# Kernel tuning notes

Hardware: AMD Instinct MI355X
Metric: run time of the kernel (lower is better)

The kernel has to match this reference:

```python
import jax, jax.numpy as jnp
import numpy as np
import math

B, DSET, DOUT, DH, H, L, M, C = 32, 512, 16, 1024, 16, 6, 127, 8
S = M + 1            # sos + maximum_components targets
DHEAD = DH // H
DIN = DSET + 1 + 2 * DOUT  # embedding input dim = 545
DTOK = 1 + 2 * DOUT        # per-step token dim = 33


def _pos_encoding(max_len, d):
    pos = np.arange(max_len, dtype=np.float32)[:, None]
    div = np.exp(np.arange(0, d, 2, dtype=np.float32) * (-math.log(10000.0) / d))
    pe = np.zeros((max_len, d), dtype=np.float32)
    pe[:, 0::2] = np.sin(pos * div)
    pe[:, 1::2] = np.cos(pos * div)
    return jnp.asarray(pe[None])  # [1, max_len, d]


def setup_inputs() -> dict:
    key = jax.random.key(0)
    ks = iter(jax.random.split(key, 64))
    def n(shape, s=0.02):
        return jax.random.normal(next(ks), shape, jnp.float32) * s
    return {
        "input": jax.random.normal(next(ks), (B, DSET), jnp.float32),
        "targets": jax.random.normal(next(ks), (B, M, DTOK), jnp.float32),
        "W_emb": n((DH, DIN)), "b_emb": jnp.zeros((DH,), jnp.float32),
        "sos": jax.random.normal(next(ks), (1, 1, DTOK), jnp.float32),
        "Wqkv": n((L, 3 * DH, DH)), "bqkv": jnp.zeros((L, 3 * DH), jnp.float32),
        "Wo": n((L, DH, DH)), "bo": jnp.zeros((L, DH), jnp.float32),
        "W1": n((L, DH, DH)), "b1": jnp.zeros((L, DH), jnp.float32),
        "W2": n((L, DH, DH)), "b2": jnp.zeros((L, DH), jnp.float32),
        "g1": jnp.ones((L, DH), jnp.float32), "be1": jnp.zeros((L, DH), jnp.float32),
        "g2": jnp.ones((L, DH), jnp.float32), "be2": jnp.zeros((L, DH), jnp.float32),
        "Wm": n((1, DH)), "bm": jnp.zeros((1,), jnp.float32),
        "Wpi_m": n((C, DH)), "bpi_m": jnp.zeros((C,), jnp.float32),
        "Wmu_m": n((C * DOUT, DH)), "bmu_m": jnp.zeros((C * DOUT,), jnp.float32),
        "Wsg_m": n((C * DOUT, DH)), "bsg_m": jnp.zeros((C * DOUT,), jnp.float32),
        "Wpi_v": n((C, DH)), "bpi_v": jnp.zeros((C,), jnp.float32),
        "Wmu_v": n((C * DOUT, DH)), "bmu_v": jnp.zeros((C * DOUT,), jnp.float32),
        "Wsg_v": n((C * DOUT, DH)), "bsg_v": jnp.zeros((C * DOUT,), jnp.float32),
    }


def _ln(x, g, b, eps=1e-5):
    m = x.mean(-1, keepdims=True)
    v = ((x - m) ** 2).mean(-1, keepdims=True)
    return (x - m) / jnp.sqrt(v + eps) * g + b


def _layer(x, Wqkv, bqkv, Wo, bo, W1, b1, W2, b2, g1, be1, g2, be2, causal):
    # PyTorch TransformerEncoderLayer (post-norm, relu, dropout=0)
    qkv = x @ Wqkv.T + bqkv                       # [B,S,3*DH]
    q, k, v = jnp.split(qkv, 3, axis=-1)
    q = q.reshape(B, -1, H, DHEAD)
    k = k.reshape(B, -1, H, DHEAD)
    v = v.reshape(B, -1, H, DHEAD)
    sc = jnp.einsum('bqhd,bkhd->bhqk', q, k) / math.sqrt(DHEAD)
    sc = jnp.where(causal, sc, -1e30)
    a = jax.nn.softmax(sc, -1)
    o = jnp.einsum('bhqk,bkhd->bqhd', a, v).reshape(B, -1, DH)
    x = _ln(x + o @ Wo.T + bo, g1, be1)
    ff = jax.nn.relu(x @ W1.T + b1) @ W2.T + b2
    return _ln(x + ff, g2, be2)


def _mdn(h, Wpi, bpi, Wmu, bmu, Wsg, bsg):
    pi = jax.nn.softmax(h @ Wpi.T + bpi, -1)                      # [B,M,C]
    mu = (h @ Wmu.T + bmu).reshape(h.shape[:-1] + (C, DOUT))      # [B,M,C,DOUT]
    var = jnp.exp(h @ Wsg.T + bsg).reshape(h.shape[:-1] + (C, DOUT))
    return pi, mu, var


def reference(input, targets, W_emb, b_emb, sos, Wqkv, bqkv, Wo, bo, W1, b1, W2, b2,
              g1, be1, g2, be2, Wm, bm, Wpi_m, bpi_m, Wmu_m, bmu_m, Wsg_m, bsg_m,
              Wpi_v, bpi_v, Wmu_v, bmu_v, Wsg_v, bsg_v):
    pe = _pos_encoding(3 * M, DH)
    tokens = jnp.broadcast_to(sos, (B, 1, DTOK))
    cond = jnp.broadcast_to(input[:, None, :], (B, S, DSET))
    seq = jnp.concatenate([tokens, targets], axis=1)              # [B,S,DTOK]
    x = jnp.concatenate([cond, seq], axis=-1) @ W_emb.T + b_emb
    x = x + pe[:, :S, :]
    causal = jnp.tril(jnp.ones((S, S), bool))[None, None]
    for i in range(L):
        x = _layer(x, Wqkv[i], bqkv[i], Wo[i], bo[i], W1[i], b1[i], W2[i], b2[i],
                   g1[i], be1[i], g2[i], be2[i], causal)
    h = x[:, :-1, :]                                              # [B,M,DH]
    masks = h @ Wm.T + bm                                         # [B,M,1]
    pi_m, mu_m, var_m = _mdn(h, Wpi_m, bpi_m, Wmu_m, bmu_m, Wsg_m, bsg_m)
    pi_v, mu_v, var_v = _mdn(h, Wpi_v, bpi_v, Wmu_v, bmu_v, Wsg_v, bsg_v)
    return (pi_m, mu_m, var_m, pi_v, mu_v, var_v, masks)
```

## Files before the change

### kernel.cpp

```cpp
#include <hip/hip_runtime.h>
#include <hip/hip_bf16.h>

typedef __hip_bfloat16 bf16;
typedef __attribute__((ext_vector_type(8))) short bfrag8;
typedef __attribute__((ext_vector_type(4))) float facc4;
typedef __attribute__((ext_vector_type(4))) unsigned short us4;
typedef __attribute__((ext_vector_type(8))) unsigned short us8;
typedef __attribute__((ext_vector_type(4))) float f32x4;

#define AS1C const __attribute__((address_space(1))) void
#define AS3  __attribute__((address_space(3))) void

__device__ __forceinline__ void gload_lds16(const void* src, void* dst) {
    __builtin_amdgcn_global_load_lds((AS1C*)src, (AS3*)dst, 16, 0, 0);
}

__device__ __forceinline__ unsigned short f2bf(float f) {
    unsigned u = __float_as_uint(f);
    unsigned r = u + 0x7FFFu + ((u >> 16) & 1u);
    return (unsigned short)(r >> 16);
}
__device__ __forceinline__ float bf2f(unsigned short u) {
    return __uint_as_float((unsigned)u << 16);
}

__global__ void prep_cvt_kernel(const float* __restrict__ input, const float* __restrict__ targets,
                                const float* __restrict__ sos, const float* __restrict__ W_emb,
                                const float* __restrict__ Wm, const float* __restrict__ Wpi_m,
                                const float* __restrict__ Wmu_m, const float* __restrict__ Wsg_m,
                                const float* __restrict__ Wpi_v, const float* __restrict__ Wmu_v,
                                const float* __restrict__ Wsg_v,
                                const float* __restrict__ bm, const float* __restrict__ bpi_m,
                                const float* __restrict__ bmu_m, const float* __restrict__ bsg_m,
                                const float* __restrict__ bpi_v, const float* __restrict__ bmu_v,
                                const float* __restrict__ bsg_v,
                                const float* __restrict__ Wqkv, const float* __restrict__ Wo,
                                const float* __restrict__ W1, const float* __restrict__ W2,
                                float* __restrict__ pe, bf16* __restrict__ xin,
                                bf16* __restrict__ wemb, bf16* __restrict__ whead,
                                float* __restrict__ bhead,
                                bf16* __restrict__ wqb, bf16* __restrict__ wob,
                                bf16* __restrict__ w1b, bf16* __restrict__ w2b) {
    int bid = blockIdx.x;
    if (bid < 4608) {
        int l = bid / 768;
        int s = bid - l * 768;
        const float* src; bf16* dst;
        if (s < 384)      { src = Wqkv + (size_t)l * 3145728; dst = wqb + (size_t)l * 3145728; }
        else if (s < 512) { src = Wo + (size_t)l * 1048576; dst = wob + (size_t)l * 1048576; s -= 384; }
        else if (s < 640) { src = W1 + (size_t)l * 1048576; dst = w1b + (size_t)l * 1048576; s -= 512; }
        else              { src = W2 + (size_t)l * 1048576; dst = w2b + (size_t)l * 1048576; s -= 640; }
        size_t pbase = (size_t)s * 1024 + threadIdx.x;
#pragma unroll
        for (int it = 0; it < 4; ++it) {
            size_t o = (pbase + it * 256) * 8;
            const f32x4* p = (const f32x4*)(src + o);
            f32x4 v1 = __builtin_nontemporal_load(p);
            f32x4 v2 = __builtin_nontemporal_load(p + 1);
            us8 w8;
            w8[0] = f2bf(v1.x); w8[1] = f2bf(v1.y); w8[2] = f2bf(v1.z); w8[3] = f2bf(v1.w);
            w8[4] = f2bf(v2.x); w8[5] = f2bf(v2.y); w8[6] = f2bf(v2.z); w8[7] = f2bf(v2.w);
            *(us8*)(dst + o) = w8;
        }
    } else if (bid < 5120) {
        int idx = (bid - 4608) * 256 + threadIdx.x;
        int s = idx >> 10, c = idx & 1023;
        int i = c >> 1;
        float div = expf(-9.210340371976184f * (float)(2 * i) * (1.f / 1024.f));
        float a = (float)s * div;
        pe[idx] = (c & 1) ? cosf(a) : sinf(a);
    } else if (bid < 5120 + 4096) {
        int row = bid - 5120;
        int b = row >> 7, s = row & 127;
        for (int c = threadIdx.x; c < 576; c += 256) {
            float v = 0.f;
            if (c < 512) v = input[b * 512 + c];
            else if (c < 545) {
                int j = c - 512;
                v = (s == 0) ? sos[j] : targets[((size_t)b * 127 + (s - 1)) * 33 + j];
            }
            xin[(size_t)row * 576 + c] = __float2bfloat16(v);
        }
    } else if (bid < 5120 + 4096 + 1024) {
        int row = bid - (5120 + 4096);
        for (int c = threadIdx.x; c < 576; c += 256)
            wemb[(size_t)row * 576 + c] = __float2bfloat16(c < 545 ? W_emb[(size_t)row * 545 + c] : 0.f);
    } else {
        int r = bid - (5120 + 4096 + 1024);
        const float* wsrc = nullptr; const float* bsrc = nullptr; int off = 0;
        if (r == 0)        { wsrc = Wm;    bsrc = bm;    off = 0; }
        else if (r < 9)    { wsrc = Wpi_m; bsrc = bpi_m; off = r - 1; }
        else if (r < 137)  { wsrc = Wmu_m; bsrc = bmu_m; off = r - 9; }
        else if (r < 265)  { wsrc = Wsg_m; bsrc = bsg_m; off = r - 137; }
        else if (r < 273)  { wsrc = Wpi_v; bsrc = bpi_v; off = r - 265; }
        else if (r < 401)  { wsrc = Wmu_v; bsrc = bmu_v; off = r - 273; }
        else if (r < 529)  { wsrc = Wsg_v; bsrc = bsg_v; off = r - 401; }
        for (int c = threadIdx.x; c < 1024; c += 256)
            whead[(size_t)r * 1024 + c] = __float2bfloat16(wsrc ? wsrc[(size_t)off * 1024 + c] : 0.f);
        if (threadIdx.x == 0 && wsrc) bhead[r] = bsrc[off];
    }
}

template<int EPI, int DBUF>
__global__ __launch_bounds__(256, DBUF ? 2 : 3) void gemm_bt(
    const bf16* __restrict__ A, const bf16* __restrict__ Bw,
    float* __restrict__ Cf, bf16* __restrict__ Cb,
    const float* __restrict__ bias, const float* __restrict__ pe,
    int M, int N, int K, int lda, int ldb, int ldc, long long Az, long long Cz)
{
    __shared__ __align__(16) bf16 sA[DBUF ? 2 : 1][128 * 64];
    __shared__ __align__(16) bf16 sB[DBUF ? 2 : 1][128 * 64];
    const int t = threadIdx.x;
    const int w = t >> 6, la = t & 63;
    const int wm = (w >> 1) * 64, wn = (w & 1) * 64;
    const int m0 = blockIdx.y * 128, n0 = blockIdx.x * 128;
    const int z = blockIdx.z;
    A += (long long)z * Az;

    const int c0 = w * 64 + la;
    facc4 zero4 = {0.f, 0.f, 0.f, 0.f};
    facc4 acc[4][4];
#pragma unroll
    for (int mi = 0; mi < 4; ++mi)
#pragma unroll
        for (int ni = 0; ni < 4; ++ni) acc[mi][ni] = zero4;

    auto stage = [&](int buf, int kt) {
#pragma unroll
        for (int i = 0; i < 4; ++i) {
            int c = i * 256 + c0;
            int r = c >> 3;
            int bc = ((c & 7) * 16) ^ ((r & 7) << 4);
            gload_lds16(A + (size_t)(m0 + r) * lda + kt + (bc >> 1),
                        (char*)sA[buf] + (size_t)(i * 256 + c0) * 16);
            gload_lds16(Bw + (size_t)(n0 + r) * ldb + kt + (bc >> 1),
                        (char*)sB[buf] + (size_t)(i * 256 + c0) * 16);
        }
    };
    auto compute = [&](int buf) {
#pragma unroll
        for (int ks = 0; ks < 2; ++ks) {
            bfrag8 af[4], bfv[4];
            const int koffb = (ks * 32 + (la >> 4) * 8) * 2;
#pragma unroll
            for (int i = 0; i < 4; ++i) {
                int rowa = wm + i * 16 + (la & 15);
                af[i] = *(const bfrag8*)((const char*)sA[buf] + rowa * 128 + (koffb ^ ((rowa & 7) << 4)));
                int rowb = wn + i * 16 + (la & 15);
                bfv[i] = *(const bfrag8*)((const char*)sB[buf] + rowb * 128 + (koffb ^ ((rowb & 7) << 4)));
            }
#pragma unroll
            for (int mi = 0; mi < 4; ++mi)
#pragma unroll
                for (int ni = 0; ni < 4; ++ni)
                    acc[mi][ni] = __builtin_amdgcn_mfma_f32_16x16x32_bf16(bfv[ni], af[mi], acc[mi][ni], 0, 0, 0);
        }
    };

    const int nk = K >> 6;
    if constexpr (DBUF) {
        stage(0, 0);
        __syncthreads();
        int cur = 0;
        for (int kt = 0; kt < nk; ++kt) {
            if (kt + 1 < nk) stage(cur ^ 1, (kt + 1) << 6);
            compute(cur);
            __syncthreads();
            cur ^= 1;
        }
    } else {
        for (int kt = 0; kt < nk; ++kt) {
            stage(0, kt << 6);
            __syncthreads();
            compute(0);
            __syncthreads();
        }
    }
#pragma unroll
    for (int mi = 0; mi < 4; ++mi) {
        int row = m0 + wm + mi * 16 + (la & 15);
#pragma unroll
        for (int ni = 0; ni < 4; ++ni) {
            int colb = n0 + wn + ni * 16 + (la >> 4) * 4;
            if constexpr (EPI == 3) {
                if (row >= M) continue;
#pragma unroll
                for (int j = 0; j < 4; ++j) {
                    int col = colb + j;
                    if (col < N)
                        Cf[(size_t)z * Cz + (size_t)row * ldc + col] = acc[mi][ni][j] + bias[col];
                }
            } else {
                float4 bv = *(const float4*)(bias + colb);
                facc4 v = acc[mi][ni];
                v[0] += bv.x; v[1] += bv.y; v[2] += bv.z; v[3] += bv.w;
                size_t cidx = (size_t)row * ldc + colb;
                if constexpr (EPI == 0) {
                    us4 o; o.x = f2bf(v[0]); o.y = f2bf(v[1]); o.z = f2bf(v[2]); o.w = f2bf(v[3]);
                    *(us4*)(Cb + cidx) = o;
                } else if constexpr (EPI == 1) {
                    us4 o;
                    o.x = f2bf(v[0] > 0.f ? v[0] : 0.f); o.y = f2bf(v[1] > 0.f ? v[1] : 0.f);
                    o.z = f2bf(v[2] > 0.f ? v[2] : 0.f); o.w = f2bf(v[3] > 0.f ? v[3] : 0.f);
                    *(us4*)(Cb + cidx) = o;
                } else {
                    float4 p = *(const float4*)(pe + (size_t)(row & 127) * 1024 + colb);
                    us4 o;
                    o.x = f2bf(v[0] + p.x); o.y = f2bf(v[1] + p.y);
                    o.z = f2bf(v[2] + p.z); o.w = f2bf(v[3] + p.w);
                    *(us4*)(Cb + cidx) = o;
                }
            }
        }
    }
}

__global__ __launch_bounds__(256) void attn_fused(const bf16* __restrict__ qkv, bf16* __restrict__ obf)
{
    __shared__ __align__(16) char lds[65536];
    char* sQ  = lds;
    char* sK  = lds + 16384;
    char* sS  = lds + 32768;
    char* sVT = lds;
    float* redm = (float*)(lds + 16384);
    float* reds = (float*)(lds + 16384 + 1024);

    const int t = threadIdx.x, w = t >> 6, la = t & 63;
    const int b = blockIdx.x >> 4, h = blockIdx.x & 15;
    const size_t base = (size_t)b * 128 * 3072 + (size_t)h * 64;

#pragma unroll
    for (int i = 0; i < 4; ++i) {
        int c = i * 256 + w * 64 + la;
        int r = c >> 3;
        int bc = ((c & 7) * 16) ^ ((r & 7) << 4);
        gload_lds16(qkv + base + (size_t)r * 3072 + (bc >> 1),
                    sQ + (size_t)(i * 256 + w * 64) * 16);
        gload_lds16(qkv + base + 1024 + (size_t)r * 3072 + (bc >> 1),
                    sK + (size_t)(i * 256 + w * 64) * 16);
    }
    __syncthreads();

    const int wm = (w >> 1) * 64, wn = (w & 1) * 64;
    facc4 zero4 = {0.f, 0.f, 0.f, 0.f};
    facc4 acc[4][4];
#pragma unroll
    for (int mi = 0; mi < 4; ++mi)
#pragma unroll
        for (int ni = 0; ni < 4; ++ni) acc[mi][ni] = zero4;
#pragma unroll
    for (int ks = 0; ks < 2; ++ks) {
        bfrag8 af[4], bfv[4];
        const int koffb = (ks * 32 + (la >> 4) * 8) * 2;
#pragma unroll
        for (int i = 0; i < 4; ++i) {
            int rowa = wm + i * 16 + (la & 15);
            af[i] = *(const bfrag8*)(sQ + rowa * 128 + (koffb ^ ((rowa & 7) << 4)));
            int rowb = wn + i * 16 + (la & 15);
            bfv[i] = *(const bfrag8*)(sK + rowb * 128 + (koffb ^ ((rowb & 7) << 4)));
        }
#pragma unroll
        for (int mi = 0; mi < 4; ++mi)
#pragma unroll
            for (int ni = 0; ni < 4; ++ni)
                acc[mi][ni] = __builtin_amdgcn_mfma_f32_16x16x32_bf16(bfv[ni], af[mi], acc[mi][ni], 0, 0, 0);
    }
    __syncthreads();

#pragma unroll
    for (int i = 0; i < 4; ++i) {
        int c = i * 256 + t;
        int r = c >> 3;
        int d0 = (c & 7) * 8;
        bfrag8 vv = *(const bfrag8*)(qkv + base + 2048 + (size_t)r * 3072 + d0);
#pragma unroll
        for (int j = 0; j < 8; ++j) {
            int d = d0 + j;
            *(short*)(sVT + d * 256 + ((2 * r) ^ ((d & 7) << 4))) = vv[j];
        }
    }

    const int colh = (w & 1) * 128;
    float tmp4[4];
#pragma unroll
    for (int mi = 0; mi < 4; ++mi) {
        int q = wm + mi * 16 + (la & 15);
        float mx = -1e30f;
#pragma unroll
        for (int ni = 0; ni < 4; ++ni) {
            int kb = wn + ni * 16 + (la >> 4) * 4;
#pragma unroll
            for (int j = 0; j < 4; ++j) {
                float s = acc[mi][ni][j] * 0.125f;
                acc[mi][ni][j] = s;
                if (kb + j <= q) mx = fmaxf(mx, s);
            }
        }
        mx = fmaxf(mx, __shfl_xor(mx, 16));
        mx = fmaxf(mx, __shfl_xor(mx, 32));
        tmp4[mi] = mx;
    }
    if ((la >> 4) == 0) {
#pragma unroll
        for (int mi = 0; mi < 4; ++mi) redm[colh + wm + mi * 16 + la] = tmp4[mi];
    }
    __syncthreads();
#pragma unroll
    for (int mi = 0; mi < 4; ++mi) {
        int q = wm + mi * 16 + (la & 15);
        float m = fmaxf(redm[q], redm[128 + q]);
        float sm = 0.f;
#pragma unroll
        for (int ni = 0; ni < 4; ++ni) {
            int kb = wn + ni * 16 + (la >> 4) * 4;
#pragma unroll
            for (int j = 0; j < 4; ++j) {
                float e = (kb + j <= q) ? __expf(acc[mi][ni][j] - m) : 0.f;
                acc[mi][ni][j] = e;
                sm += e;
            }
        }
        sm += __shfl_xor(sm, 16);
        sm += __shfl_xor(sm, 32);
        tmp4[mi] = sm;
    }
    __syncthreads();
    if ((la >> 4) == 0) {
#pragma unroll
        for (int mi = 0; mi < 4; ++mi) reds[colh + wm + mi * 16 + la] = tmp4[mi];
    }
    __syncthreads();
#pragma unroll
    for (int mi = 0; mi < 4; ++mi) {
        int q = wm + mi * 16 + (la & 15);
        float inv = 1.f / (reds[q] + reds[128 + q]);
#pragma unroll
        for (int ni = 0; ni < 4; ++ni) {
            int kb = wn + ni * 16 + (la >> 4) * 4;
            us4 sv;
            sv.x = f2bf(acc[mi][ni][0] * inv); sv.y = f2bf(acc[mi][ni][1] * inv);
            sv.z = f2bf(acc[mi][ni][2] * inv); sv.w = f2bf(acc[mi][ni][3] * inv);
            *(us4*)(sS + q * 256 + ((2 * kb) ^ ((q & 7) << 4))) = sv;
        }
    }
    __syncthreads();

    const int wm2 = (w >> 1) * 64, wn2 = (w & 1) * 32;
    facc4 a2[4][2];
#pragma unroll
    for (int mi = 0; mi < 4; ++mi) { a2[mi][0] = zero4; a2[mi][1] = zero4; }
#pragma unroll
    for (int ks = 0; ks < 4; ++ks) {
        bfrag8 pa[4], vb[2];
        const int koffb = (ks * 32 + (la >> 4) * 8) * 2;
#pragma unroll
        for (int mi = 0; mi < 4; ++mi) {
            int rowa = wm2 + mi * 16 + (la & 15);
            pa[mi] = *(const bfrag8*)(sS + rowa * 256 + (koffb ^ ((rowa & 7) << 4)));
        }
#pragma unroll
        for (int ni = 0; ni < 2; ++ni) {
            int rowb = wn2 + ni * 16 + (la & 15);
            vb[ni] = *(const bfrag8*)(sVT + rowb * 256 + (koffb ^ ((rowb & 7) << 4)));
        }
#pragma unroll
        for (int mi = 0; mi < 4; ++mi)
#pragma unroll
            for (int ni = 0; ni < 2; ++ni)
                a2[mi][ni] = __builtin_amdgcn_mfma_f32_16x16x32_bf16(vb[ni], pa[mi], a2[mi][ni], 0, 0, 0);
    }
#pragma unroll
    for (int mi = 0; mi < 4; ++mi) {
        int s = wm2 + mi * 16 + (la & 15);
#pragma unroll
        for (int ni = 0; ni < 2; ++ni) {
            int db = wn2 + ni * 16 + (la >> 4) * 4;
            us4 ov;
            ov.x = f2bf(a2[mi][ni][0]); ov.y = f2bf(a2[mi][ni][1]);
            ov.z = f2bf(a2[mi][ni][2]); ov.w = f2bf(a2[mi][ni][3]);
            *(us4*)(obf + ((size_t)(b * 128 + s)) * 1024 + h * 64 + db) = ov;
        }
    }
}

__global__ __launch_bounds__(256) void ln_res_kernel(const bf16* __restrict__ go,
                                                     const bf16* __restrict__ res,
                                                     const float* __restrict__ g, const float* __restrict__ be,
                                                     bf16* __restrict__ xb_out)
{
    const int row = blockIdx.x, t = threadIdx.x;
    size_t o = (size_t)row * 1024 + t * 4;
    us4 gv4 = *(const us4*)(go + o);
    us4 rv4 = *(const us4*)(res + o);
    float t0 = bf2f(rv4.x) + bf2f(gv4.x);
    float t1 = bf2f(rv4.y) + bf2f(gv4.y);
    float t2 = bf2f(rv4.z) + bf2f(gv4.z);
    float t3 = bf2f(rv4.w) + bf2f(gv4.w);
    float s = t0 + t1 + t2 + t3;
    float q = t0 * t0 + t1 * t1 + t2 * t2 + t3 * t3;
#pragma unroll
    for (int off = 32; off; off >>= 1) {
        s += __shfl_xor(s, off);
        q += __shfl_xor(q, off);
    }
    __shared__ float ssum[4], sqs[4];
    if ((t & 63) == 0) { ssum[t >> 6] = s; sqs[t >> 6] = q; }
    __syncthreads();
    s = ssum[0] + ssum[1] + ssum[2] + ssum[3];
    q = sqs[0] + sqs[1] + sqs[2] + sqs[3];
    float mean = s * (1.f / 1024.f);
    float var = q * (1.f / 1024.f) - mean * mean;
    float rstd = rsqrtf(var + 1e-5f);
    float4 gv = *(const float4*)(g + t * 4);
    float4 bv = *(const float4*)(be + t * 4);
    float o0 = (t0 - mean) * rstd * gv.x + bv.x;
    float o1 = (t1 - mean) * rstd * gv.y + bv.y;
    float o2 = (t2 - mean) * rstd * gv.z + bv.z;
    float o3 = (t3 - mean) * rstd * gv.w + bv.w;
    us4 obv; obv.x = f2bf(o0); obv.y = f2bf(o1); obv.z = f2bf(o2); obv.w = f2bf(o3);
    *(us4*)(xb_out + o) = obv;
}

__global__ void finalize_kernel(const float* __restrict__ hout, float* __restrict__ out) {
    const size_t O_PI_M = 0, O_MU_M = 32512, O_VAR_M = 552704, O_PI_V = 1072896,
                 O_MU_V = 1105408, O_VAR_V = 1625600, O_MASK = 2145792;
    int rm = blockIdx.x;
    const float* hrow = hout + (size_t)rm * 529;
    int t = threadIdx.x;
    if (t < 128) {
        out[O_MU_M  + (size_t)rm * 128 + t] = hrow[9 + t];
        out[O_VAR_M + (size_t)rm * 128 + t] = expf(hrow[137 + t]);
        out[O_MU_V  + (size_t)rm * 128 + t] = hrow[273 + t];
        out[O_VAR_V + (size_t)rm * 128 + t] = expf(hrow[401 + t]);
    } else if (t == 128) {
        out[O_MASK + rm] = hrow[0];
    } else if (t == 129 || t == 130) {
        int boff = (t == 129) ? 1 : 265;
        size_t oo = ((t == 129) ? O_PI_M : O_PI_V) + (size_t)rm * 8;
        float v[8], mx = -1e30f;
#pragma unroll
        for (int j = 0; j < 8; ++j) { v[j] = hrow[boff + j]; mx = fmaxf(mx, v[j]); }
        float sm = 0.f;
#pragma unroll
        for (int j = 0; j < 8; ++j) { v[j] = expf(v[j] - mx); sm += v[j]; }
        float inv = 1.f / sm;
#pragma unroll
        for (int j = 0; j < 8; ++j) out[oo + j] = v[j] * inv;
    }
}

extern "C" void kernel_launch(void* const* d_in, const int* in_sizes, int n_in,
                              void* d_out, int out_size, void* d_ws, size_t ws_size,
                              hipStream_t stream) {
    (void)in_sizes; (void)n_in; (void)out_size; (void)ws_size;
    const float* input   = (const float*)d_in[0];
    const float* targets = (const float*)d_in[1];
    const float* W_emb   = (const float*)d_in[2];
    const float* b_emb   = (const float*)d_in[3];
    const float* sos     = (const float*)d_in[4];
    const float* Wqkv    = (const float*)d_in[5];
    const float* bqkv    = (const float*)d_in[6];
    const float* Wo      = (const float*)d_in[7];
    const float* bo      = (const float*)d_in[8];
    const float* W1      = (const float*)d_in[9];
    const float* b1      = (const float*)d_in[10];
    const float* W2      = (const float*)d_in[11];
    const float* b2      = (const float*)d_in[12];
    const float* g1      = (const float*)d_in[13];
    const float* be1     = (const float*)d_in[14];
    const float* g2      = (const float*)d_in[15];
    const float* be2     = (const float*)d_in[16];
    const float* Wm      = (const float*)d_in[17];
    const float* bm      = (const float*)d_in[18];
    const float* Wpi_m   = (const float*)d_in[19];
    const float* bpi_m   = (const float*)d_in[20];
    const float* Wmu_m   = (const float*)d_in[21];
    const float* bmu_m   = (const float*)d_in[22];
    const float* Wsg_m   = (const float*)d_in[23];
    const float* bsg_m   = (const float*)d_in[24];
    const float* Wpi_v   = (const float*)d_in[25];
    const float* bpi_v   = (const float*)d_in[26];
    const float* Wmu_v   = (const float*)d_in[27];
    const float* bmu_v   = (const float*)d_in[28];
    const float* Wsg_v   = (const float*)d_in[29];
    const float* bsg_v   = (const float*)d_in[30];
    float* out = (float*)d_out;

    char* ws = (char*)d_ws;
    float* pe      = (float*)(ws + 0);
    bf16*  xin     = (bf16*)(ws + 524288);
    bf16*  wemb    = (bf16*)(ws + 5242880);
    bf16*  whead   = (bf16*)(ws + 6422528);
    float* bhead   = (float*)(ws + 7733248);
    bf16*  xb      = (bf16*)(ws + 24513024);
    bf16*  qkvb    = (bf16*)(ws + 32901632);
    bf16*  ob      = (bf16*)(ws + 58067456);
    bf16*  tmpb    = (bf16*)(ws + 66456064);
    bf16*  wqb_all = (bf16*)(ws + 83233280);
    bf16*  wob_all = (bf16*)(ws + 120982016);
    bf16*  w1b_all = (bf16*)(ws + 133564928);
    bf16*  w2b_all = (bf16*)(ws + 146147840);
    float* hout    = (float*)(ws + 158730752);

    prep_cvt_kernel<<<10880, 256, 0, stream>>>(input, targets, sos, W_emb,
                                               Wm, Wpi_m, Wmu_m, Wsg_m, Wpi_v, Wmu_v, Wsg_v,
                                               bm, bpi_m, bmu_m, bsg_m, bpi_v, bmu_v, bsg_v,
                                               Wqkv, Wo, W1, W2,
                                               pe, xin, wemb, whead, bhead,
                                               wqb_all, wob_all, w1b_all, w2b_all);
    gemm_bt<4, 1><<<dim3(8, 32, 1), 256, 0, stream>>>(xin, wemb, nullptr, xb, b_emb, pe,
                                                      4096, 1024, 576, 576, 576, 1024, 0, 0);
    for (int l = 0; l < 6; ++l) {
        const bf16* wqb = wqb_all + (size_t)l * 3145728;
        const bf16* wob = wob_all + (size_t)l * 1048576;
        const bf16* w1b = w1b_all + (size_t)l * 1048576;
        const bf16* w2b = w2b_all + (size_t)l * 1048576;
        gemm_bt<0, 0><<<dim3(24, 32, 1), 256, 0, stream>>>(xb, wqb, nullptr, qkvb, bqkv + l * 3072,
                                                           nullptr, 4096, 3072, 1024, 1024, 1024, 3072, 0, 0);
        attn_fused<<<512, 256, 0, stream>>>(qkvb, ob);
        gemm_bt<0, 1><<<dim3(8, 32, 1), 256, 0, stream>>>(ob, wob, nullptr, tmpb, bo + l * 1024,
                                                          nullptr, 4096, 1024, 1024, 1024, 1024, 1024, 0, 0);
        ln_res_kernel<<<4096, 256, 0, stream>>>(tmpb, xb, g1 + l * 1024, be1 + l * 1024, xb);
        gemm_bt<1, 1><<<dim3(8, 32, 1), 256, 0, stream>>>(xb, w1b, nullptr, ob, b1 + l * 1024,
                                                          nullptr, 4096, 1024, 1024, 1024, 1024, 1024, 0, 0);
        gemm_bt<0, 1><<<dim3(8, 32, 1), 256, 0, stream>>>(ob, w2b, nullptr, tmpb, b2 + l * 1024,
                                                          nullptr, 4096, 1024, 1024, 1024, 1024, 1024, 0, 0);
        ln_res_kernel<<<4096, 256, 0, stream>>>(tmpb, xb, g2 + l * 1024, be2 + l * 1024, xb);
    }
    gemm_bt<3, 1><<<dim3(5, 1, 32), 256, 0, stream>>>(xb, whead, hout, nullptr, bhead, nullptr,
                                                      127, 529, 1024, 1024, 1024, 529, 131072LL, 67183LL);
    finalize_kernel<<<4064, 256, 0, stream>>>(hout, out);
}
```

Baseline: 773.9 us.

## Use 512-thread blocks for double-buffered GEMMs and vectorize prep conversion

The double-buffered GEMM now runs 8 waves per 128x128 tile instead of 4. Each wave owns a 32x64 sub-tile, and each thread stages half as many LDS chunks. This is meant to raise latency hiding and the number of active waves per CU for the N=1024 GEMMs, which launch only 256 blocks. The prep kernel is also reworked to do vectorized 8-wide bf16 conversion with fewer blocks and a single block for the head biases, cutting per-element scalar work. More waves per tile means each wave reuses fewer A fragments, so LDS read traffic per MFMA goes up.

```diff
diff --git a/kernel.cpp b/kernel.cpp
--- a/kernel.cpp
+++ b/kernel.cpp
@@ -42,6 +42,7 @@
                                 bf16* __restrict__ wqb, bf16* __restrict__ wob,
                                 bf16* __restrict__ w1b, bf16* __restrict__ w2b) {
     int bid = blockIdx.x;
+    int t = threadIdx.x;
     if (bid < 4608) {
         int l = bid / 768;
         int s = bid - l * 768;
@@ -50,7 +51,7 @@
         else if (s < 512) { src = Wo + (size_t)l * 1048576; dst = wob + (size_t)l * 1048576; s -= 384; }
         else if (s < 640) { src = W1 + (size_t)l * 1048576; dst = w1b + (size_t)l * 1048576; s -= 512; }
         else              { src = W2 + (size_t)l * 1048576; dst = w2b + (size_t)l * 1048576; s -= 640; }
-        size_t pbase = (size_t)s * 1024 + threadIdx.x;
+        size_t pbase = (size_t)s * 1024 + t;
 #pragma unroll
         for (int it = 0; it < 4; ++it) {
             size_t o = (pbase + it * 256) * 8;
@@ -62,95 +63,150 @@
             w8[4] = f2bf(v2.x); w8[5] = f2bf(v2.y); w8[6] = f2bf(v2.z); w8[7] = f2bf(v2.w);
             *(us8*)(dst + o) = w8;
         }
-    } else if (bid < 5120) {
-        int idx = (bid - 4608) * 256 + threadIdx.x;
-        int s = idx >> 10, c = idx & 1023;
-        int i = c >> 1;
-        float div = expf(-9.210340371976184f * (float)(2 * i) * (1.f / 1024.f));
-        float a = (float)s * div;
-        pe[idx] = (c & 1) ? cosf(a) : sinf(a);
-    } else if (bid < 5120 + 4096) {
-        int row = bid - 5120;
+    } else if (bid < 4736) {
+        int s = bid - 4608;
+        float4 v;
+#pragma unroll
+        for (int j = 0; j < 4; ++j) {
+            int c = t * 4 + j;
+            int i = c >> 1;
+            float div = expf(-9.210340371976184f * (float)(2 * i) * (1.f / 1024.f));
+            float a = (float)s * div;
+            v[j] = (c & 1) ? cosf(a) : sinf(a);
+        }
+        *(float4*)(pe + (size_t)s * 1024 + t * 4) = v;
+    } else if (bid < 5888) {
+        int chunk = (bid - 4736) * 256 + t;
+        int row = chunk / 72;
+        int cc = chunk - row * 72;
         int b = row >> 7, s = row & 127;
-        for (int c = threadIdx.x; c < 576; c += 256) {
-            float v = 0.f;
-            if (c < 512) v = input[b * 512 + c];
-            else if (c < 545) {
-                int j = c - 512;
-                v = (s == 0) ? sos[j] : targets[((size_t)b * 127 + (s - 1)) * 33 + j];
+        us8 w8;
+        if (cc < 64) {
+            const float* p = input + (size_t)b * 512 + cc * 8;
+            float4 v1 = *(const float4*)p;
+            float4 v2 = *(const float4*)(p + 4);
+            w8[0] = f2bf(v1.x); w8[1] = f2bf(v1.y); w8[2] = f2bf(v1.z); w8[3] = f2bf(v1.w);
+            w8[4] = f2bf(v2.x); w8[5] = f2bf(v2.y); w8[6] = f2bf(v2.z); w8[7] = f2bf(v2.w);
+        } else {
+#pragma unroll
+            for (int j = 0; j < 8; ++j) {
+                int col = cc * 8 + j;
+                float v = 0.f;
+                if (col < 545) {
+                    int jj = col - 512;
+                    v = (s == 0) ? sos[jj] : targets[((size_t)b * 127 + (s - 1)) * 33 + jj];
+                }
+                w8[j] = f2bf(v);
             }
-            xin[(size_t)row * 576 + c] = __float2bfloat16(v);
-        }
-    } else if (bid < 5120 + 4096 + 1024) {
-        int row = bid - (5120 + 4096);
-        for (int c = threadIdx.x; c < 576; c += 256)
-            wemb[(size_t)row * 576 + c] = __float2bfloat16(c < 545 ? W_emb[(size_t)row * 545 + c] : 0.f);
+        }
+        *(us8*)(xin + (size_t)row * 576 + cc * 8) = w8;
+    } else if (bid < 6176) {
+        int chunk = (bid - 5888) * 256 + t;
+        int row = chunk / 72;
+        int cc = chunk - row * 72;
+        us8 w8;
+#pragma unroll
+        for (int j = 0; j < 8; ++j) {
+            int col = cc * 8 + j;
+            w8[j] = f2bf(col < 545 ? W_emb[(size_t)row * 545 + col] : 0.f);
+        }
+        *(us8*)(wemb + (size_t)row * 576 + cc * 8) = w8;
+    } else if (bid < 6496) {
+        int chunk = (bid - 6176) * 256 + t;
+        int r = chunk >> 7;
+        int cc = chunk & 127;
+        const float* wsrc = nullptr; int off = 0;
+        if (r == 0)        { wsrc = Wm;    off = 0; }
+        else if (r < 9)    { wsrc = Wpi_m; off = r - 1; }
+        else if (r < 137)  { wsrc = Wmu_m; off = r - 9; }
+        else if (r < 265)  { wsrc = Wsg_m; off = r - 137; }
+        else if (r < 273)  { wsrc = Wpi_v; off = r - 265; }
+        else if (r < 401)  { wsrc = Wmu_v; off = r - 273; }
+        else if (r < 529)  { wsrc = Wsg_v; off = r - 401; }
+        us8 w8;
+        if (wsrc) {
+            const float* p = wsrc + (size_t)off * 1024 + cc * 8;
+            float4 v1 = *(const float4*)p;
+            float4 v2 = *(const float4*)(p + 4);
+            w8[0] = f2bf(v1.x); w8[1] = f2bf(v1.y); w8[2] = f2bf(v1.z); w8[3] = f2bf(v1.w);
+            w8[4] = f2bf(v2.x); w8[5] = f2bf(v2.y); w8[6] = f2bf(v2.z); w8[7] = f2bf(v2.w);
+        } else {
+#pragma unroll
+            for (int j = 0; j < 8; ++j) w8[j] = 0;
+        }
+        *(us8*)(whead + (size_t)r * 1024 + cc * 8) = w8;
     } else {
-        int r = bid - (5120 + 4096 + 1024);
-        const float* wsrc = nullptr; const float* bsrc = nullptr; int off = 0;
-        if (r == 0)        { wsrc = Wm;    bsrc = bm;    off = 0; }
-        else if (r < 9)    { wsrc = Wpi_m; bsrc = bpi_m; off = r - 1; }
-        else if (r < 137)  { wsrc = Wmu_m; bsrc = bmu_m; off = r - 9; }
-        else if (r < 265)  { wsrc = Wsg_m; bsrc = bsg_m; off = r - 137; }
-        else if (r < 273)  { wsrc = Wpi_v; bsrc = bpi_v; off = r - 265; }
-        else if (r < 401)  { wsrc = Wmu_v; bsrc = bmu_v; off = r - 273; }
-        else if (r < 529)  { wsrc = Wsg_v; bsrc = bsg_v; off = r - 401; }
-        for (int c = threadIdx.x; c < 1024; c += 256)
-            whead[(size_t)r * 1024 + c] = __float2bfloat16(wsrc ? wsrc[(size_t)off * 1024 + c] : 0.f);
-        if (threadIdx.x == 0 && wsrc) bhead[r] = bsrc[off];
-    }
-}
-
-template<int EPI, int DBUF>
-__global__ __launch_bounds__(256, DBUF ? 2 : 3) void gemm_bt(
+        if (t < 529) {
+            const float* bsrc; int off;
+            if (t == 0)       { bsrc = bm;    off = 0; }
+            else if (t < 9)   { bsrc = bpi_m; off = t - 1; }
+            else if (t < 137) { bsrc = bmu_m; off = t - 9; }
+            else if (t < 265) { bsrc = bsg_m; off = t - 137; }
+            else if (t < 273) { bsrc = bpi_v; off = t - 265; }
+            else if (t < 401) { bsrc = bmu_v; off = t - 273; }
+            else              { bsrc = bsg_v; off = t - 401; }
+            bhead[t] = bsrc[off];
+        }
+    }
+}
+
+template<int EPI, int CFG>
+__global__ __launch_bounds__(CFG ? 512 : 256, CFG ? 2 : 3) void gemm_bt(
     const bf16* __restrict__ A, const bf16* __restrict__ Bw,
     float* __restrict__ Cf, bf16* __restrict__ Cb,
     const float* __restrict__ bias, const float* __restrict__ pe,
     int M, int N, int K, int lda, int ldb, int ldc, long long Az, long long Cz)
 {
-    __shared__ __align__(16) bf16 sA[DBUF ? 2 : 1][128 * 64];
-    __shared__ __align__(16) bf16 sB[DBUF ? 2 : 1][128 * 64];
+    constexpr int NT = CFG ? 512 : 256;
+    constexpr int NB = CFG ? 2 : 1;
+    constexpr int MI = CFG ? 2 : 4;
+    constexpr int NCH = 1024 / NT;
+    __shared__ __align__(16) bf16 sA[NB][128 * 64];
+    __shared__ __align__(16) bf16 sB[NB][128 * 64];
     const int t = threadIdx.x;
     const int w = t >> 6, la = t & 63;
-    const int wm = (w >> 1) * 64, wn = (w & 1) * 64;
+    const int wm = CFG ? (w >> 1) * 32 : (w >> 1) * 64;
+    const int wn = (w & 1) * 64;
     const int m0 = blockIdx.y * 128, n0 = blockIdx.x * 128;
     const int z = blockIdx.z;
     A += (long long)z * Az;
 
-    const int c0 = w * 64 + la;
     facc4 zero4 = {0.f, 0.f, 0.f, 0.f};
-    facc4 acc[4][4];
-#pragma unroll
-    for (int mi = 0; mi < 4; ++mi)
+    facc4 acc[MI][4];
+#pragma unroll
+    for (int mi = 0; mi < MI; ++mi)
 #pragma unroll
         for (int ni = 0; ni < 4; ++ni) acc[mi][ni] = zero4;
 
     auto stage = [&](int buf, int kt) {
 #pragma unroll
-        for (int i = 0; i < 4; ++i) {
-            int c = i * 256 + c0;
+        for (int i = 0; i < NCH; ++i) {
+            int c = i * NT + t;
             int r = c >> 3;
             int bc = ((c & 7) * 16) ^ ((r & 7) << 4);
             gload_lds16(A + (size_t)(m0 + r) * lda + kt + (bc >> 1),
-                        (char*)sA[buf] + (size_t)(i * 256 + c0) * 16);
+                        (char*)sA[buf] + (size_t)c * 16);
             gload_lds16(Bw + (size_t)(n0 + r) * ldb + kt + (bc >> 1),
-                        (char*)sB[buf] + (size_t)(i * 256 + c0) * 16);
+                        (char*)sB[buf] + (size_t)c * 16);
         }
     };
     auto compute = [&](int buf) {
 #pragma unroll
         for (int ks = 0; ks < 2; ++ks) {
-            bfrag8 af[4], bfv[4];
+            bfrag8 af[MI], bfv[4];
             const int koffb = (ks * 32 + (la >> 4) * 8) * 2;
 #pragma unroll
-            for (int i = 0; i < 4; ++i) {
+            for (int i = 0; i < MI; ++i) {
                 int rowa = wm + i * 16 + (la & 15);
                 af[i] = *(const bfrag8*)((const char*)sA[buf] + rowa * 128 + (koffb ^ ((rowa & 7) << 4)));
+            }
+#pragma unroll
+            for (int i = 0; i < 4; ++i) {
                 int rowb = wn + i * 16 + (la & 15);
                 bfv[i] = *(const bfrag8*)((const char*)sB[buf] + rowb * 128 + (koffb ^ ((rowb & 7) << 4)));
             }
 #pragma unroll
-            for (int mi = 0; mi < 4; ++mi)
+            for (int mi = 0; mi < MI; ++mi)
 #pragma unroll
                 for (int ni = 0; ni < 4; ++ni)
                     acc[mi][ni] = __builtin_amdgcn_mfma_f32_16x16x32_bf16(bfv[ni], af[mi], acc[mi][ni], 0, 0, 0);
@@ -158,7 +214,7 @@
     };
 
     const int nk = K >> 6;
-    if constexpr (DBUF) {
+    if constexpr (CFG) {
         stage(0, 0);
         __syncthreads();
         int cur = 0;
@@ -177,7 +233,7 @@
         }
     }
 #pragma unroll
-    for (int mi = 0; mi < 4; ++mi) {
+    for (int mi = 0; mi < MI; ++mi) {
         int row = m0 + wm + mi * 16 + (la & 15);
 #pragma unroll
         for (int ni = 0; ni < 4; ++ni) {
@@ -502,13 +558,13 @@
     bf16*  w2b_all = (bf16*)(ws + 146147840);
     float* hout    = (float*)(ws + 158730752);
 
-    prep_cvt_kernel<<<10880, 256, 0, stream>>>(input, targets, sos, W_emb,
-                                               Wm, Wpi_m, Wmu_m, Wsg_m, Wpi_v, Wmu_v, Wsg_v,
-                                               bm, bpi_m, bmu_m, bsg_m, bpi_v, bmu_v, bsg_v,
-                                               Wqkv, Wo, W1, W2,
-                                               pe, xin, wemb, whead, bhead,
-                                               wqb_all, wob_all, w1b_all, w2b_all);
-    gemm_bt<4, 1><<<dim3(8, 32, 1), 256, 0, stream>>>(xin, wemb, nullptr, xb, b_emb, pe,
+    prep_cvt_kernel<<<6497, 256, 0, stream>>>(input, targets, sos, W_emb,
+                                              Wm, Wpi_m, Wmu_m, Wsg_m, Wpi_v, Wmu_v, Wsg_v,
+                                              bm, bpi_m, bmu_m, bsg_m, bpi_v, bmu_v, bsg_v,
+                                              Wqkv, Wo, W1, W2,
+                                              pe, xin, wemb, whead, bhead,
+                                              wqb_all, wob_all, w1b_all, w2b_all);
+    gemm_bt<4, 1><<<dim3(8, 32, 1), 512, 0, stream>>>(xin, wemb, nullptr, xb, b_emb, pe,
                                                       4096, 1024, 576, 576, 576, 1024, 0, 0);
     for (int l = 0; l < 6; ++l) {
         const bf16* wqb = wqb_all + (size_t)l * 3145728;
@@ -518,16 +574,16 @@
         gemm_bt<0, 0><<<dim3(24, 32, 1), 256, 0, stream>>>(xb, wqb, nullptr, qkvb, bqkv + l * 3072,
                                                            nullptr, 4096, 3072, 1024, 1024, 1024, 3072, 0, 0);
         attn_fused<<<512, 256, 0, stream>>>(qkvb, ob);
-        gemm_bt<0, 1><<<dim3(8, 32, 1), 256, 0, stream>>>(ob, wob, nullptr, tmpb, bo + l * 1024,
+        gemm_bt<0, 1><<<dim3(8, 32, 1), 512, 0, stream>>>(ob, wob, nullptr, tmpb, bo + l * 1024,
                                                           nullptr, 4096, 1024, 1024, 1024, 1024, 1024, 0, 0);
         ln_res_kernel<<<4096, 256, 0, stream>>>(tmpb, xb, g1 + l * 1024, be1 + l * 1024, xb);
-        gemm_bt<1, 1><<<dim3(8, 32, 1), 256, 0, stream>>>(xb, w1b, nullptr, ob, b1 + l * 1024,
+        gemm_bt<1, 1><<<dim3(8, 32, 1), 512, 0, stream>>>(xb, w1b, nullptr, ob, b1 + l * 1024,
                                                           nullptr, 4096, 1024, 1024, 1024, 1024, 1024, 0, 0);
-        gemm_bt<0, 1><<<dim3(8, 32, 1), 256, 0, stream>>>(ob, w2b, nullptr, tmpb, b2 + l * 1024,
+        gemm_bt<0, 1><<<dim3(8, 32, 1), 512, 0, stream>>>(ob, w2b, nullptr, tmpb, b2 + l * 1024,
                                                           nullptr, 4096, 1024, 1024, 1024, 1024, 1024, 0, 0);
         ln_res_kernel<<<4096, 256, 0, stream>>>(tmpb, xb, g2 + l * 1024, be2 + l * 1024, xb);
     }
-    gemm_bt<3, 1><<<dim3(5, 1, 32), 256, 0, stream>>>(xb, whead, hout, nullptr, bhead, nullptr,
+    gemm_bt<3, 1><<<dim3(5, 1, 32), 512, 0, stream>>>(xb, whead, hout, nullptr, bhead, nullptr,
                                                       127, 529, 1024, 1024, 1024, 529, 131072LL, 67183LL);
     finalize_kernel<<<4064, 256, 0, stream>>>(hout, out);
 }
```

Measured after the change: 766.4 us. About the same (-1.0%).
